# Performance work log

Measured on AMD Instinct MI355X. Metric: run time of the kernel, lower is better.

## Reference

```python
import jax, jax.numpy as jnp
import numpy as np
from jax import lax

NUM_HEADS = 8
HEAD_DIM = 32
DIM = NUM_HEADS * HEAD_DIM  # 256
SR = 2
B, H, W = 4, 64, 64


def setup_inputs() -> dict:
    key = jax.random.key(0)
    ks = jax.random.split(key, 6)
    x = jax.random.normal(ks[0], (B, DIM, H, W), dtype=jnp.float32)
    # query: 1x1 conv without bias -> plain [out,in] matrix
    Wq = jax.random.normal(ks[1], (DIM, DIM), dtype=jnp.float32) * (1.0 / np.sqrt(DIM))
    # key/value: sr x sr conv, stride sr, no bias (OIHW)
    Wk = jax.random.normal(ks[2], (DIM, DIM, SR, SR), dtype=jnp.float32) * (1.0 / np.sqrt(DIM * SR * SR))
    Wv = jax.random.normal(ks[3], (DIM, DIM, SR, SR), dtype=jnp.float32) * (1.0 / np.sqrt(DIM * SR * SR))
    rel_h = jax.random.normal(ks[4], (1, NUM_HEADS, HEAD_DIM, 1, H // SR), dtype=jnp.float32)
    rel_w = jax.random.normal(ks[5], (1, NUM_HEADS, HEAD_DIM, W // SR, 1), dtype=jnp.float32)
    return {"x": x, "Wq": Wq, "Wk": Wk, "Wv": Wv, "rel_h": rel_h, "rel_w": rel_w}


def reference(x, Wq, Wk, Wv, rel_h, rel_w):
    b, c, h, w = x.shape
    nh, hd = NUM_HEADS, HEAD_DIM
    scale = hd ** (-0.5)
    dn = ('NCHW', 'OIHW', 'NCHW')

    # q: 1x1 conv == channel matmul; [B, C, H*W] -> [B, nh, hd, Nq]
    q = jnp.einsum('oc,bchw->bohw', Wq, x).reshape(b, nh, hd, h * w)
    # k, v: sr x sr conv, stride sr -> [B, nh, hd, Nkv]
    k = lax.conv_general_dilated(x, Wk, window_strides=(SR, SR), padding='VALID',
                                 dimension_numbers=dn).reshape(b, nh, hd, -1)
    v = lax.conv_general_dilated(x, Wv, window_strides=(SR, SR), padding='VALID',
                                 dimension_numbers=dn).reshape(b, nh, hd, -1)

    # attn scores: q^T k -> [B, nh, Nq, Nkv]
    attn = jnp.einsum('bhdn,bhdm->bhnm', q, k)
    # relative positional bias: (rel_h + rel_w) broadcast -> [nh, hd, Nkv]
    pos = (rel_h + rel_w).reshape(nh, hd, -1)
    attn = attn + jnp.einsum('bhdn,hdm->bhnm', q, pos)
    attn = jax.nn.softmax(attn * scale, axis=-1)

    # out = v @ attn^T -> [B, nh, hd, Nq] -> [B, C, H, W]
    out = jnp.einsum('bhdm,bhnm->bhdn', v, attn).reshape(b, c, h, w)
    return out
```

## Files before the change

kernel.cpp:

```cpp
#include <hip/hip_runtime.h>
#include <math.h>


typedef __bf16 bf16;
typedef __attribute__((ext_vector_type(4))) __bf16 bf16x4;
typedef __attribute__((ext_vector_type(8))) __bf16 bf16x8;
typedef __attribute__((ext_vector_type(4))) float f32x4;
typedef __attribute__((ext_vector_type(2))) __fp16 fp16x2_raw;
typedef __attribute__((ext_vector_type(4))) _Float16 f16x4;

#define MFMA16 __builtin_amdgcn_mfma_f32_16x16x32_bf16
#define MFMA16H __builtin_amdgcn_mfma_f32_16x16x16f16

#define QSCALE 0.25503486f
#define SOFTMAX_SHIFT 10.0f

__global__ void k_prep_w(const float* __restrict__ Wq, const float* __restrict__ Wk,
                         const float* __restrict__ Wv,
                         bf16* __restrict__ Wq_bf, bf16* __restrict__ Wkv_bf) {
    int tid = blockIdx.x * 256 + threadIdx.x;
    int c = tid >> 8, i = tid & 255;
    const float* Wsrc = (c < 256) ? Wk : Wv;
    int cs = c & 255;
    f32x4 w4 = ((const f32x4*)Wsrc)[cs * 256 + i];
#pragma unroll
    for (int tap = 0; tap < 4; tap++)
        Wkv_bf[c * 1024 + tap * 256 + i] = (bf16)w4[tap];
    if (tid < 16384) {
        f32x4 q4 = ((const f32x4*)Wq)[tid];
        bf16x4 o;
#pragma unroll
        for (int e = 0; e < 4; e++) o[e] = (bf16)(q4[e] * QSCALE);
        *(bf16x4*)(Wq_bf + tid * 4) = o;
    }
}

__global__ void k_xT(const float* __restrict__ x, bf16* __restrict__ xT) {
    int b = blockIdx.z, c0 = blockIdx.y * 64, n0 = blockIdx.x * 64;
    __shared__ float tile[64][65];
    int t = threadIdx.x;
    const float* xp = x + (size_t)(b * 256 + c0) * 4096 + n0;
#pragma unroll
    for (int k2 = 0; k2 < 16; k2++) {
        int flat = k2 * 256 + t;
        int row = flat >> 6, col = flat & 63;
        tile[row][col] = xp[(size_t)row * 4096 + col];
    }
    __syncthreads();
    bf16* op = xT + (size_t)(b * 4096 + n0) * 256 + c0;
#pragma unroll
    for (int k2 = 0; k2 < 16; k2++) {
        int flat = k2 * 256 + t;
        int row = flat >> 6, col = flat & 63;
        op[(size_t)row * 256 + col] = (bf16)tile[col][row];
    }
}

__launch_bounds__(256)
__global__ void k_gemm_kv(const bf16* __restrict__ xT, const bf16* __restrict__ Wkv_bf,
                          const float* __restrict__ rel_h, const float* __restrict__ rel_w,
                          bf16* __restrict__ kpos_t, _Float16* __restrict__ v_td) {
    int b = blockIdx.z;
    int bx = blockIdx.x;
    int m0 = bx * 32;
    int c0w = blockIdx.y * 64 + (threadIdx.x >> 6) * 16;
    int t = threadIdx.x, l = t & 63;
    int lr = l & 15, lg = l >> 4;
    __shared__ __align__(16) bf16 Ps[2][32 * 264];
    const bf16* xb = xT + (size_t)b * 4096 * 256;
    int srow = t >> 3;
    int scu0 = (t & 7) * 4;
    uint4 pre[4];
#define LOAD_CHUNK(tap)                                                        \
    {                                                                          \
        int dy = (tap) >> 1, dx = (tap) & 1;                                   \
        const bf16* src = xb + (size_t)((2 * bx + dy) * 64 + 2 * srow + dx) * 256; \
        _Pragma("unroll")                                                      \
        for (int j = 0; j < 4; j++)                                            \
            pre[j] = *(const uint4*)(src + (scu0 + j) * 8);                    \
    }
#define WRITE_CHUNK(buf)                                                       \
    {                                                                          \
        bf16* dst = Ps[buf] + srow * 264 + scu0 * 8;                           \
        _Pragma("unroll")                                                      \
        for (int j = 0; j < 4; j++) *(uint4*)(dst + j * 8) = pre[j];           \
    }
    LOAD_CHUNK(0)
    WRITE_CHUNK(0)
    const bf16* Gkb = Wkv_bf + (size_t)(c0w + lr) * 1024 + lg * 8;
    const bf16* Gvb = Gkb + 256 * 1024;
    f32x4 accK[2] = {}, accV[2] = {};
    for (int ch = 0; ch < 4; ch++) {
        if (ch < 3) LOAD_CHUNK(ch + 1)
        __syncthreads();
        const bf16* P = Ps[ch & 1];
#pragma unroll
        for (int kk = 0; kk < 8; kk++) {
            bf16x8 pa0 = *(const bf16x8*)(P + lr * 264 + kk * 32 + lg * 8);
            bf16x8 pa1 = *(const bf16x8*)(P + (16 + lr) * 264 + kk * 32 + lg * 8);
            bf16x8 gk = *(const bf16x8*)(Gkb + ch * 256 + kk * 32);
            bf16x8 gv = *(const bf16x8*)(Gvb + ch * 256 + kk * 32);
            accK[0] = MFMA16(pa0, gk, accK[0], 0, 0, 0);
            accK[1] = MFMA16(pa1, gk, accK[1], 0, 0, 0);
            accV[0] = MFMA16(gv, pa0, accV[0], 0, 0, 0);
            accV[1] = MFMA16(gv, pa1, accV[1], 0, 0, 0);
        }
        if (ch < 3) {
            __syncthreads();
            WRITE_CHUNK((ch + 1) & 1)
        }
    }
    {
        int cc = c0w + lr;
        float rw = rel_w[cc * 32 + bx];
#pragma unroll
        for (int i = 0; i < 2; i++)
#pragma unroll
            for (int r = 0; r < 4; r++) {
                int ml = i * 16 + lg * 4 + r;
                float val = accK[i][r] + rw + rel_h[cc * 32 + ml];
                kpos_t[((size_t)(b * 8 + (cc >> 5)) * 1024 + m0 + ml) * 32 + (cc & 31)] = (bf16)val;
            }
    }
#pragma unroll
    for (int j = 0; j < 2; j++) {
        int m = m0 + j * 16 + lr;
#pragma unroll
        for (int r = 0; r < 4; r++) {
            int cc = c0w + lg * 4 + r;
            v_td[((size_t)(b * 8 + (cc >> 5)) * 32 + (cc & 31)) * 1024 + m] = (_Float16)accV[j][r];
        }
    }
#undef LOAD_CHUNK
#undef WRITE_CHUNK
}

__launch_bounds__(512, 8)
__global__ void k_attn(const bf16* __restrict__ xT, const bf16* __restrict__ Wq_bf,
                       const bf16* __restrict__ kpos_t, const _Float16* __restrict__ v_td,
                       float* __restrict__ out) {
    int b = blockIdx.z, h = blockIdx.y;
    int t = threadIdx.x;
    int w = t >> 6, l = t & 63;
    int n0 = blockIdx.x * 128 + w * 16;
    int lr = l & 15, lg = l >> 4;
    const size_t bh = (size_t)(b * 8 + h);
    __shared__ __align__(16) char smem[2 * 128 * 32 * 2 + 2 * 32 * 136 * 2];
    bf16* KsB = (bf16*)smem;
    _Float16* VsB = (_Float16*)(smem + 16384);
    const bf16* Kb = kpos_t + bh * 1024 * 32;
    const _Float16* Vb = v_td + bh * 32 * 1024;
    uint4 pk_r, pv_r;
#define LOADCH(ch)                                                             \
    {                                                                          \
        pk_r = ((const uint4*)(Kb + (size_t)(ch) * 128 * 32))[t];              \
        pv_r = *(const uint4*)(Vb + (size_t)(t >> 4) * 1024 + (ch) * 128 +     \
                               (t & 15) * 8);                                  \
    }
#define WRITECH(buf)                                                           \
    {                                                                          \
        int m = t >> 2;                                                        \
        int phys = ((m >> 1) + (t & 3)) & 3;                                   \
        *(uint4*)(&KsB[(buf) * 4096 + m * 32 + phys * 8]) = pk_r;              \
        *(uint4*)(&VsB[(buf) * (32 * 136) + (t >> 4) * 136 + (t & 15) * 8]) = pv_r; \
    }
    LOADCH(0)
    bf16* Qs = (bf16*)smem + w * 1280;
    bf16x8 bq0;
    {
        const bf16* Aw = Wq_bf + (size_t)(h * 32 + lr) * 256 + lg * 8;
        const bf16* Bx = xT + (size_t)(b * 4096 + n0 + lr) * 256 + lg * 8;
        f32x4 aq[2] = {};
#pragma unroll
        for (int kk = 0; kk < 8; kk++) {
            bf16x8 a0 = *(const bf16x8*)(Aw + kk * 32);
            bf16x8 a1 = *(const bf16x8*)(Aw + 16 * 256 + kk * 32);
            bf16x8 b0 = *(const bf16x8*)(Bx + kk * 32);
            aq[0] = MFMA16(a0, b0, aq[0], 0, 0, 0);
            aq[1] = MFMA16(a1, b0, aq[1], 0, 0, 0);
        }
#pragma unroll
        for (int i = 0; i < 2; i++) {
            bf16x4 pk;
#pragma unroll
            for (int r = 0; r < 4; r++) pk[r] = (bf16)aq[i][r];
            *(bf16x4*)(Qs + lr * 40 + i * 16 + lg * 4) = pk;
        }
        bf16x4 a0 = *(const bf16x4*)(Qs + lr * 40 + lg * 8);
        bf16x4 a1 = *(const bf16x4*)(Qs + lr * 40 + lg * 8 + 4);
#pragma unroll
        for (int e = 0; e < 4; e++) { bq0[e] = a0[e]; bq0[4 + e] = a1[e]; }
    }
    __syncthreads();
    WRITECH(0)
    LOADCH(1)
    __syncthreads();
    f32x4 accO[2] = {};
    f32x4 accS = {};
    const f16x4 onesv = {(_Float16)1.f, (_Float16)1.f, (_Float16)1.f, (_Float16)1.f};
    const f32x4 zs = {-SOFTMAX_SHIFT, -SOFTMAX_SHIFT, -SOFTMAX_SHIFT, -SOFTMAX_SHIFT};
    const int koff = (((lr >> 1) + lg) & 3) * 8;
    for (int ch = 0; ch < 8; ch++) {
        const bf16* Kc = KsB + (ch & 1) * 4096;
        const _Float16* Vc = VsB + (ch & 1) * (32 * 136);
        __builtin_amdgcn_s_setprio(1);
#pragma unroll
        for (int tt = 0; tt < 8; tt++) {
            bf16x8 ak = *(const bf16x8*)(Kc + (tt * 16 + lr) * 32 + koff);
            f32x4 s0 = MFMA16(ak, bq0, zs, 0, 0, 0);
            f16x4 p0;
            {
                fp16x2_raw c01 = __builtin_amdgcn_cvt_pkrtz(
                    __builtin_amdgcn_exp2f(s0[0]), __builtin_amdgcn_exp2f(s0[1]));
                fp16x2_raw c23 = __builtin_amdgcn_cvt_pkrtz(
                    __builtin_amdgcn_exp2f(s0[2]), __builtin_amdgcn_exp2f(s0[3]));
                p0[0] = c01[0]; p0[1] = c01[1]; p0[2] = c23[0]; p0[3] = c23[1];
            }
            f16x4 v0 = *(const f16x4*)(Vc + lr * 136 + tt * 16 + lg * 4);
            f16x4 v1 = *(const f16x4*)(Vc + (16 + lr) * 136 + tt * 16 + lg * 4);
            accO[0] = MFMA16H(p0, v0, accO[0], 0, 0, 0);
            accO[1] = MFMA16H(p0, v1, accO[1], 0, 0, 0);
            accS    = MFMA16H(p0, onesv, accS, 0, 0, 0);
        }
        __builtin_amdgcn_s_setprio(0);
        if (ch < 7) {
            WRITECH((ch + 1) & 1)
            if (ch < 6) LOADCH(ch + 2)
            __syncthreads();
        }
    }
#undef LOADCH
#undef WRITECH
    float inv[4];
#pragma unroll
    for (int r = 0; r < 4; r++) inv[r] = 1.0f / accS[r];
#pragma unroll
    for (int dt = 0; dt < 2; dt++) {
        int c = h * 32 + dt * 16 + lr;
        float* op = out + (size_t)(b * 256 + c) * 4096 + n0 + lg * 4;
        f32x4 o;
#pragma unroll
        for (int r = 0; r < 4; r++) o[r] = accO[dt][r] * inv[r];
        *(f32x4*)op = o;
    }
}

extern "C" void kernel_launch(void* const* d_in, const int* in_sizes, int n_in,
                              void* d_out, int out_size, void* d_ws, size_t ws_size,
                              hipStream_t stream) {
    const float* x    = (const float*)d_in[0];
    const float* Wq   = (const float*)d_in[1];
    const float* Wk   = (const float*)d_in[2];
    const float* Wv   = (const float*)d_in[3];
    const float* relh = (const float*)d_in[4];
    const float* relw = (const float*)d_in[5];
    float* out = (float*)d_out;
    char* ws = (char*)d_ws;

    bf16*      xT     = (bf16*)(ws);
    bf16*      kposT  = (bf16*)(ws + (8u << 20));
    _Float16*  v_td   = (_Float16*)(ws + (10u << 20));
    bf16*      Wq_bf  = (bf16*)(ws + (12u << 20));
    bf16*      Wkv_bf = (bf16*)(ws + (12u << 20) + (256u << 10));

    k_prep_w <<<512,            256, 0, stream>>>(Wq, Wk, Wv, Wq_bf, Wkv_bf);
    k_xT     <<<dim3(64, 4, 4), 256, 0, stream>>>(x, xT);
    k_gemm_kv<<<dim3(32, 4, 4), 256, 0, stream>>>(xT, Wkv_bf, relh, relw, kposT, v_td);
    k_attn   <<<dim3(32, 8, 4), 512, 0, stream>>>(xT, Wq_bf, kposT, v_td, out);
}
```

Baseline: 146.5 us.

## Vectorize weight prep and transpose, pad V smem, batch QK MFMAs before exp

Weight prep now has each thread handle four input columns and write bf16x4 stores, so the grid shrinks to 192 blocks. The x transpose uses float4 global loads and bf16x8 stores. In the attention kernel the V shared-memory row stride changes from 136 to 140 halves to alter the bank mapping. The inner loop also now issues four QK MFMAs before the exps and the PV MFMAs, to hide MFMA latency at the cost of more live registers.

```diff
diff --git a/kernel.cpp b/kernel.cpp
--- a/kernel.cpp
+++ b/kernel.cpp
@@ -14,24 +14,34 @@
 
 #define QSCALE 0.25503486f
 #define SOFTMAX_SHIFT 10.0f
+#define VSTR 140
 
 __global__ void k_prep_w(const float* __restrict__ Wq, const float* __restrict__ Wk,
                          const float* __restrict__ Wv,
                          bf16* __restrict__ Wq_bf, bf16* __restrict__ Wkv_bf) {
     int tid = blockIdx.x * 256 + threadIdx.x;
-    int c = tid >> 8, i = tid & 255;
-    const float* Wsrc = (c < 256) ? Wk : Wv;
-    int cs = c & 255;
-    f32x4 w4 = ((const f32x4*)Wsrc)[cs * 256 + i];
-#pragma unroll
-    for (int tap = 0; tap < 4; tap++)
-        Wkv_bf[c * 1024 + tap * 256 + i] = (bf16)w4[tap];
-    if (tid < 16384) {
-        f32x4 q4 = ((const f32x4*)Wq)[tid];
+    if (tid < 32768) {
+        int c = tid >> 6, i4 = (tid & 63) * 4;
+        const float* Wsrc = (c < 256) ? Wk : Wv;
+        int cs = c & 255;
+        f32x4 r[4];
+#pragma unroll
+        for (int j = 0; j < 4; j++)
+            r[j] = ((const f32x4*)Wsrc)[cs * 256 + i4 + j];
+#pragma unroll
+        for (int tap = 0; tap < 4; tap++) {
+            bf16x4 o;
+#pragma unroll
+            for (int j = 0; j < 4; j++) o[j] = (bf16)r[j][tap];
+            *(bf16x4*)(Wkv_bf + c * 1024 + tap * 256 + i4) = o;
+        }
+    } else {
+        int q = tid - 32768;
+        f32x4 q4 = ((const f32x4*)Wq)[q];
         bf16x4 o;
 #pragma unroll
         for (int e = 0; e < 4; e++) o[e] = (bf16)(q4[e] * QSCALE);
-        *(bf16x4*)(Wq_bf + tid * 4) = o;
+        *(bf16x4*)(Wq_bf + q * 4) = o;
     }
 }
 
@@ -41,18 +51,23 @@
     int t = threadIdx.x;
     const float* xp = x + (size_t)(b * 256 + c0) * 4096 + n0;
 #pragma unroll
-    for (int k2 = 0; k2 < 16; k2++) {
-        int flat = k2 * 256 + t;
-        int row = flat >> 6, col = flat & 63;
-        tile[row][col] = xp[(size_t)row * 4096 + col];
+    for (int it = 0; it < 4; it++) {
+        int u = it * 256 + t;
+        int row = u >> 4, colq = u & 15;
+        f32x4 v = *(const f32x4*)(xp + (size_t)row * 4096 + colq * 4);
+#pragma unroll
+        for (int e = 0; e < 4; e++) tile[row][colq * 4 + e] = v[e];
     }
     __syncthreads();
     bf16* op = xT + (size_t)(b * 4096 + n0) * 256 + c0;
 #pragma unroll
-    for (int k2 = 0; k2 < 16; k2++) {
-        int flat = k2 * 256 + t;
-        int row = flat >> 6, col = flat & 63;
-        op[(size_t)row * 256 + col] = (bf16)tile[col][row];
+    for (int it = 0; it < 2; it++) {
+        int u = it * 256 + t;
+        int orow = u >> 3, oc8 = (u & 7) * 8;
+        bf16x8 o;
+#pragma unroll
+        for (int e = 0; e < 8; e++) o[e] = (bf16)tile[oc8 + e][orow];
+        *(bf16x8*)(op + (size_t)orow * 256 + oc8) = o;
     }
 }
 
@@ -145,7 +160,7 @@
     int n0 = blockIdx.x * 128 + w * 16;
     int lr = l & 15, lg = l >> 4;
     const size_t bh = (size_t)(b * 8 + h);
-    __shared__ __align__(16) char smem[2 * 128 * 32 * 2 + 2 * 32 * 136 * 2];
+    __shared__ __align__(16) char smem[16384 + 2 * 32 * VSTR * 2];
     bf16* KsB = (bf16*)smem;
     _Float16* VsB = (_Float16*)(smem + 16384);
     const bf16* Kb = kpos_t + bh * 1024 * 32;
@@ -162,7 +177,7 @@
         int m = t >> 2;                                                        \
         int phys = ((m >> 1) + (t & 3)) & 3;                                   \
         *(uint4*)(&KsB[(buf) * 4096 + m * 32 + phys * 8]) = pk_r;              \
-        *(uint4*)(&VsB[(buf) * (32 * 136) + (t >> 4) * 136 + (t & 15) * 8]) = pv_r; \
+        *(uint4*)(&VsB[(buf) * (32 * VSTR) + (t >> 4) * VSTR + (t & 15) * 8]) = pv_r; \
     }
     LOADCH(0)
     bf16* Qs = (bf16*)smem + w * 1280;
@@ -202,25 +217,35 @@
     const int koff = (((lr >> 1) + lg) & 3) * 8;
     for (int ch = 0; ch < 8; ch++) {
         const bf16* Kc = KsB + (ch & 1) * 4096;
-        const _Float16* Vc = VsB + (ch & 1) * (32 * 136);
+        const _Float16* Vc = VsB + (ch & 1) * (32 * VSTR);
         __builtin_amdgcn_s_setprio(1);
 #pragma unroll
-        for (int tt = 0; tt < 8; tt++) {
-            bf16x8 ak = *(const bf16x8*)(Kc + (tt * 16 + lr) * 32 + koff);
-            f32x4 s0 = MFMA16(ak, bq0, zs, 0, 0, 0);
-            f16x4 p0;
-            {
+        for (int half = 0; half < 2; half++) {
+            f32x4 s[4];
+#pragma unroll
+            for (int i = 0; i < 4; i++) {
+                int tt = half * 4 + i;
+                bf16x8 ak = *(const bf16x8*)(Kc + (tt * 16 + lr) * 32 + koff);
+                s[i] = MFMA16(ak, bq0, zs, 0, 0, 0);
+            }
+            f16x4 p[4];
+#pragma unroll
+            for (int i = 0; i < 4; i++) {
                 fp16x2_raw c01 = __builtin_amdgcn_cvt_pkrtz(
-                    __builtin_amdgcn_exp2f(s0[0]), __builtin_amdgcn_exp2f(s0[1]));
+                    __builtin_amdgcn_exp2f(s[i][0]), __builtin_amdgcn_exp2f(s[i][1]));
                 fp16x2_raw c23 = __builtin_amdgcn_cvt_pkrtz(
-                    __builtin_amdgcn_exp2f(s0[2]), __builtin_amdgcn_exp2f(s0[3]));
-                p0[0] = c01[0]; p0[1] = c01[1]; p0[2] = c23[0]; p0[3] = c23[1];
-            }
-            f16x4 v0 = *(const f16x4*)(Vc + lr * 136 + tt * 16 + lg * 4);
-            f16x4 v1 = *(const f16x4*)(Vc + (16 + lr) * 136 + tt * 16 + lg * 4);
-            accO[0] = MFMA16H(p0, v0, accO[0], 0, 0, 0);
-            accO[1] = MFMA16H(p0, v1, accO[1], 0, 0, 0);
-            accS    = MFMA16H(p0, onesv, accS, 0, 0, 0);
+                    __builtin_amdgcn_exp2f(s[i][2]), __builtin_amdgcn_exp2f(s[i][3]));
+                p[i][0] = c01[0]; p[i][1] = c01[1]; p[i][2] = c23[0]; p[i][3] = c23[1];
+            }
+#pragma unroll
+            for (int i = 0; i < 4; i++) {
+                int tt = half * 4 + i;
+                f16x4 v0 = *(const f16x4*)(Vc + lr * VSTR + tt * 16 + lg * 4);
+                f16x4 v1 = *(const f16x4*)(Vc + (16 + lr) * VSTR + tt * 16 + lg * 4);
+                accO[0] = MFMA16H(p[i], v0, accO[0], 0, 0, 0);
+                accO[1] = MFMA16H(p[i], v1, accO[1], 0, 0, 0);
+                accS    = MFMA16H(p[i], onesv, accS, 0, 0, 0);
+            }
         }
         __builtin_amdgcn_s_setprio(0);
         if (ch < 7) {
@@ -263,7 +288,7 @@
     bf16*      Wq_bf  = (bf16*)(ws + (12u << 20));
     bf16*      Wkv_bf = (bf16*)(ws + (12u << 20) + (256u << 10));
 
-    k_prep_w <<<512,            256, 0, stream>>>(Wq, Wk, Wv, Wq_bf, Wkv_bf);
+    k_prep_w <<<192,            256, 0, stream>>>(Wq, Wk, Wv, Wq_bf, Wkv_bf);
     k_xT     <<<dim3(64, 4, 4), 256, 0, stream>>>(x, xT);
     k_gemm_kv<<<dim3(32, 4, 4), 256, 0, stream>>>(xT, Wkv_bf, relh, relw, kposT, v_td);
     k_attn   <<<dim3(32, 8, 4), 512, 0, stream>>>(xT, Wq_bf, kposT, v_td, out);
```

After: 161.6 us. +10.4%, slower.
